# Kernel optimization log

Hardware: AMD Instinct MI355X
Metric: run time of the kernel (lower is better)

The kernel has to match this reference:

```python
import jax, jax.numpy as jnp
import numpy as np

EPS = 1e-8
TEMPERATURE = 1.0  # e0_T, no epoch scaling applied at construction
LABEL_SMOOTH = 0.05


def setup_inputs() -> dict:
    key = jax.random.key(0)
    k1, k2 = jax.random.split(key)
    B, C, H, W = 16, 19, 512, 512
    logits = jax.random.normal(k1, (B, C, H, W), dtype=jnp.float32)
    targets = jax.random.randint(k2, (B, H, W), 0, C, dtype=jnp.int64)
    # confusion matrix initialized as in EMloss.__init__
    off = np.log((LABEL_SMOOTH + EPS) / (C - 1))
    cm = np.full((C, C), off, dtype=np.float32)
    np.fill_diagonal(cm, np.log(1.0 - LABEL_SMOOTH + EPS))
    confusion_matrix = jnp.asarray(cm)
    return {"logits": logits, "targets": targets, "confusion_matrix": confusion_matrix}


def reference(logits, targets, confusion_matrix):
    # temperature softmax over class dim (dim=1); mathematically identical to
    # the original exp(x/T)/sum(exp(x/T)) but numerically stable
    pred = jax.nn.softmax(logits / TEMPERATURE, axis=1)          # [B,C,H,W]
    ncm = jax.nn.softmax(confusion_matrix, axis=1)               # [C,C]
    # pre_p[b,c,h,w] = ncm[c, targets[b,h,w]]  (fused gather over whole batch)
    pre_p = jnp.take(ncm, targets, axis=1)                        # [C,B,H,W]
    pre_p = jnp.transpose(pre_p, (1, 0, 2, 3))                    # [B,C,H,W]
    numel_p = pre_p * pred                                        # [B,C,H,W]
    # q is detached in the original (detach().clone())
    q = jax.lax.stop_gradient(numel_p / numel_p.sum(axis=1, keepdims=True))
    # freeze_confusion=False branch: q * (log(pre_p+eps) + log(pred+eps))
    img_loss = (q * (jnp.log(pre_p + EPS) + jnp.log(pred + EPS))).sum(axis=1)  # [B,H,W]
    per_image = img_loss.mean(axis=(1, 2))                        # [B]
    batch_loss = -per_image.mean()
    return pred, batch_loss
```

## Files before the change

### kernel.cpp

```cpp
#include <hip/hip_runtime.h>

#define EPS 1e-8f

constexpr int B = 16, C = 19, H = 512, W = 512;
constexpr int HW = H * W;
constexpr int NPIX = B * HW;
constexpr long long NPRED = (long long)B * C * HW;


__global__ void ncm_kernel(const float* __restrict__ cm, float* __restrict__ ws) {
    int t = threadIdx.x;
    if (t == 0) ws[768] = 0.0f;
    if (t < C) {
        float row[C];
        float m = -1e30f;
        #pragma unroll
        for (int j = 0; j < C; ++j) { row[j] = cm[t * C + j]; m = fmaxf(m, row[j]); }
        float s = 0.0f;
        #pragma unroll
        for (int j = 0; j < C; ++j) { row[j] = __expf(row[j] - m); s += row[j]; }
        float inv = 1.0f / s;
        #pragma unroll
        for (int j = 0; j < C; ++j) {
            float v = row[j] * inv;
            ws[t * C + j] = v;
            ws[361 + t * C + j] = __logf(v + EPS);
        }
    }
}

__global__ __launch_bounds__(256) void emloss_main(
        const float* __restrict__ logits,
        const int* __restrict__ targets,
        const float* __restrict__ ws,
        float* __restrict__ pred,
        float* __restrict__ loss_acc) {
    __shared__ float s_ncm[C * C];
    __shared__ float s_lpre[C * C];
    for (int i = threadIdx.x; i < C * C; i += blockDim.x) {
        s_ncm[i]  = ws[i];
        s_lpre[i] = ws[361 + i];
    }
    __syncthreads();

    int g = blockIdx.x * blockDim.x + threadIdx.x;
    int pbase = g * 4;
    int b = pbase / HW;
    int r = pbase - b * HW;
    const float* lp = logits + (size_t)b * C * HW + r;
    float*       op = pred   + (size_t)b * C * HW + r;

    float xs[C][4];
    #pragma unroll
    for (int c = 0; c < C; ++c) {
        float4 v = *(const float4*)(lp + (size_t)c * HW);
        xs[c][0] = v.x; xs[c][1] = v.y; xs[c][2] = v.z; xs[c][3] = v.w;
    }
    int4 tv = *(const int4*)(targets + pbase);
    int tt[4] = {tv.x, tv.y, tv.z, tv.w};

    float inv_s[4];
    #pragma unroll
    for (int k = 0; k < 4; ++k) {
        float m = -1e30f;
        #pragma unroll
        for (int c = 0; c < C; ++c) m = fmaxf(m, xs[c][k]);
        float s = 0.0f;
        #pragma unroll
        for (int c = 0; c < C; ++c) {
            float e = __expf(xs[c][k] - m);
            xs[c][k] = e;
            s += e;
        }
        inv_s[k] = 1.0f / s;
    }

    float denom[4] = {0, 0, 0, 0};
    float wsum[4]  = {0, 0, 0, 0};
    #pragma unroll
    for (int c = 0; c < C; ++c) {
        float pk[4];
        #pragma unroll
        for (int k = 0; k < 4; ++k) {
            float p = xs[c][k] * inv_s[k];
            pk[k] = p;
            float nm  = s_ncm[c * C + tt[k]];
            float num = nm * p;
            denom[k] += num;
            wsum[k]  += num * (s_lpre[c * C + tt[k]] + __logf(p + EPS));
        }
        float4 pv = make_float4(pk[0], pk[1], pk[2], pk[3]);
        *(float4*)(op + (size_t)c * HW) = pv;
    }

    float lsum = 0.0f;
    #pragma unroll
    for (int k = 0; k < 4; ++k) lsum += wsum[k] / denom[k];

    #pragma unroll
    for (int off = 32; off > 0; off >>= 1) lsum += __shfl_down(lsum, off);
    if ((threadIdx.x & 63) == 0) atomicAdd(loss_acc, lsum);
}

__global__ void finalize_kernel(const float* __restrict__ acc, float* __restrict__ out) {
    out[0] = -acc[0] / (float)NPIX;
}

extern "C" void kernel_launch(void* const* d_in, const int* in_sizes, int n_in,
                              void* d_out, int out_size, void* d_ws, size_t ws_size,
                              hipStream_t stream) {
    const float* logits  = (const float*)d_in[0];
    const int*   targets = (const int*)d_in[1];
    const float* cm      = (const float*)d_in[2];
    float* out = (float*)d_out;
    float* ws  = (float*)d_ws;

    hipLaunchKernelGGL(ncm_kernel, dim3(1), dim3(64), 0, stream, cm, ws);

    int groups = NPIX / 4;
    int block = 256;
    int grid = groups / block;
    hipLaunchKernelGGL(emloss_main, dim3(grid), dim3(block), 0, stream,
                       logits, targets, ws, out, ws + 768);

    hipLaunchKernelGGL(finalize_kernel, dim3(1), dim3(1), 0, stream,
                       ws + 768, out + NPRED);
}
```

Baseline: 617.0 us.

## Halve pixels per thread and compute log-softmax algebraically instead of per-element logs

Each thread now handles two pixels instead of four, and the kernel asks for higher occupancy via launch bounds. The per-class log(p+eps) is replaced by (x - max) minus a single log of the sum, which removes most transcendental calls. Probability writes are deferred to a second pass, and the wave partial sums are combined in shared memory so only one atomic per block is issued. The risks are narrower float2 memory accesses and the small numerical difference from dropping eps inside the log.

```diff
diff --git a/kernel.cpp b/kernel.cpp
--- a/kernel.cpp
+++ b/kernel.cpp
@@ -29,7 +29,7 @@
     }
 }
 
-__global__ __launch_bounds__(256) void emloss_main(
+__global__ __launch_bounds__(256, 6) void emloss_main(
         const float* __restrict__ logits,
         const int* __restrict__ targets,
         const float* __restrict__ ws,
@@ -37,6 +37,7 @@
         float* __restrict__ loss_acc) {
     __shared__ float s_ncm[C * C];
     __shared__ float s_lpre[C * C];
+    __shared__ float s_red[4];
     for (int i = threadIdx.x; i < C * C; i += blockDim.x) {
         s_ncm[i]  = ws[i];
         s_lpre[i] = ws[361 + i];
@@ -44,62 +45,61 @@
     __syncthreads();
 
     int g = blockIdx.x * blockDim.x + threadIdx.x;
-    int pbase = g * 4;
-    int b = pbase / HW;
-    int r = pbase - b * HW;
+    int pbase = g * 2;
+    int b = pbase >> 18;
+    int r = pbase & (HW - 1);
     const float* lp = logits + (size_t)b * C * HW + r;
     float*       op = pred   + (size_t)b * C * HW + r;
 
-    float xs[C][4];
+    float xs[C][2];
     #pragma unroll
     for (int c = 0; c < C; ++c) {
-        float4 v = *(const float4*)(lp + (size_t)c * HW);
-        xs[c][0] = v.x; xs[c][1] = v.y; xs[c][2] = v.z; xs[c][3] = v.w;
+        float2 v = *(const float2*)(lp + (size_t)c * HW);
+        xs[c][0] = v.x; xs[c][1] = v.y;
     }
-    int4 tv = *(const int4*)(targets + pbase);
-    int tt[4] = {tv.x, tv.y, tv.z, tv.w};
+    int2 tv = *(const int2*)(targets + pbase);
+    int tt[2] = {tv.x, tv.y};
 
-    float inv_s[4];
+    float m[2] = {-1e30f, -1e30f};
     #pragma unroll
-    for (int k = 0; k < 4; ++k) {
-        float m = -1e30f;
-        #pragma unroll
-        for (int c = 0; c < C; ++c) m = fmaxf(m, xs[c][k]);
-        float s = 0.0f;
-        #pragma unroll
-        for (int c = 0; c < C; ++c) {
-            float e = __expf(xs[c][k] - m);
-            xs[c][k] = e;
-            s += e;
-        }
-        inv_s[k] = 1.0f / s;
+    for (int c = 0; c < C; ++c) {
+        m[0] = fmaxf(m[0], xs[c][0]);
+        m[1] = fmaxf(m[1], xs[c][1]);
     }
 
-    float denom[4] = {0, 0, 0, 0};
-    float wsum[4]  = {0, 0, 0, 0};
+    float s[2]     = {0.0f, 0.0f};
+    float denom[2] = {0.0f, 0.0f};
+    float acc[2]   = {0.0f, 0.0f};
     #pragma unroll
     for (int c = 0; c < C; ++c) {
-        float pk[4];
         #pragma unroll
-        for (int k = 0; k < 4; ++k) {
-            float p = xs[c][k] * inv_s[k];
-            pk[k] = p;
-            float nm  = s_ncm[c * C + tt[k]];
-            float num = nm * p;
+        for (int k = 0; k < 2; ++k) {
+            float d = xs[c][k] - m[k];
+            float e = __expf(d);
+            s[k] += e;
+            float num = s_ncm[c * C + tt[k]] * e;
             denom[k] += num;
-            wsum[k]  += num * (s_lpre[c * C + tt[k]] + __logf(p + EPS));
+            acc[k]   += num * (s_lpre[c * C + tt[k]] + d);
+            xs[c][k] = e;
         }
-        float4 pv = make_float4(pk[0], pk[1], pk[2], pk[3]);
-        *(float4*)(op + (size_t)c * HW) = pv;
     }
 
-    float lsum = 0.0f;
+    float inv0 = 1.0f / s[0], inv1 = 1.0f / s[1];
     #pragma unroll
-    for (int k = 0; k < 4; ++k) lsum += wsum[k] / denom[k];
+    for (int c = 0; c < C; ++c) {
+        float2 pv = make_float2(xs[c][0] * inv0, xs[c][1] * inv1);
+        *(float2*)(op + (size_t)c * HW) = pv;
+    }
+
+    float lsum = (acc[0] / denom[0] - __logf(s[0]))
+               + (acc[1] / denom[1] - __logf(s[1]));
 
     #pragma unroll
     for (int off = 32; off > 0; off >>= 1) lsum += __shfl_down(lsum, off);
-    if ((threadIdx.x & 63) == 0) atomicAdd(loss_acc, lsum);
+    if ((threadIdx.x & 63) == 0) s_red[threadIdx.x >> 6] = lsum;
+    __syncthreads();
+    if (threadIdx.x == 0)
+        atomicAdd(loss_acc, s_red[0] + s_red[1] + s_red[2] + s_red[3]);
 }
 
 __global__ void finalize_kernel(const float* __restrict__ acc, float* __restrict__ out) {
@@ -117,7 +117,7 @@
 
     hipLaunchKernelGGL(ncm_kernel, dim3(1), dim3(64), 0, stream, cm, ws);
 
-    int groups = NPIX / 4;
+    int groups = NPIX / 2;
     int block = 256;
     int grid = groups / block;
     hipLaunchKernelGGL(emloss_main, dim3(grid), dim3(block), 0, stream,
```

New measurement: 529.6 us. -14.2%, faster.
